# Optimization experiments

Hardware: AMD Instinct MI355X
Metric: run time of the kernel (lower is better)

Reference implementation:

```python
import jax, jax.numpy as jnp
import numpy as np

GAMMA = 0.3
R_PERCENT = 0.2
LAMBDA_PENALTY = 0.5
EPS = 1e-06

B_SZ, N_HEADS, K_FULL = 16, 32, 32768
K_IMG = 16384


def _zscore(x):
    mu = x.mean(axis=-1, keepdims=True)
    std = jnp.sqrt(((x - mu) ** 2).mean(axis=-1, keepdims=True))  # unbiased=False
    return (x - mu) / (std + EPS)


def _topk_binary(scores, k):
    # scores: [B,H] -> binary mask [B,H]; only strictly-positive topk values count
    vals, idx = jax.lax.top_k(scores, k)
    b = jnp.arange(scores.shape[0])[:, None]
    return jnp.zeros_like(scores).at[b, idx].set((vals > 0).astype(scores.dtype))


def setup_inputs() -> dict:
    key = jax.random.key(0)
    k1, k2, k3, k4, k5 = jax.random.split(key, 5)
    attn_logits_last = jax.random.normal(k1, (B_SZ, N_HEADS, K_FULL), dtype=jnp.float32)
    # exactly K_IMG image tokens per row (alternating pattern -> strided gather)
    image_mask = jnp.tile((jnp.arange(K_FULL) % 2 == 0).astype(jnp.int32)[None, :], (B_SZ, 1))
    feat_C = jax.random.normal(k2, (B_SZ, K_IMG), dtype=jnp.float32)
    feat_A = jax.random.normal(k3, (B_SZ, K_IMG), dtype=jnp.float32)
    feat_D = jax.random.normal(k4, (B_SZ, K_IMG), dtype=jnp.float32)
    feat_B = jax.random.normal(k5, (B_SZ, K_IMG), dtype=jnp.float32)
    return {"attn_logits_last": attn_logits_last, "image_mask": image_mask,
            "feat_C": feat_C, "feat_A": feat_A, "feat_D": feat_D, "feat_B": feat_B}


def reference(attn_logits_last, image_mask, feat_C, feat_A, feat_D, feat_B):
    B, H, K_full = attn_logits_last.shape
    K_img = feat_C.shape[1]

    # --- compute_rf ---
    C_t = jax.nn.relu(_zscore(feat_C))
    A_t = jax.nn.sigmoid(_zscore(feat_A))
    D_t = jax.nn.sigmoid(_zscore(feat_D))
    B_t = jax.nn.sigmoid(_zscore(feat_B))
    denom = jnp.maximum(1.0 + LAMBDA_PENALTY * (D_t + B_t), EPS)
    rf = jnp.maximum(C_t * A_t / denom, 0.0)  # [B,K_img]

    # --- align: positions of image tokens (exactly K_img ones per row) ---
    idx = jax.vmap(lambda m: jnp.nonzero(m, size=K_img)[0])(image_mask)  # [B,K_img]

    # --- image-normalized attention ---
    probs_full = jax.nn.softmax(attn_logits_last, axis=-1)
    mask_f = image_mask[:, None, :].astype(attn_logits_last.dtype)  # [B,1,K_full]
    probs_img = probs_full * mask_f
    probs_img_norm = probs_img / jnp.maximum(probs_img.sum(axis=-1, keepdims=True), EPS)
    attn_img_norm = jnp.take_along_axis(probs_img_norm, idx[:, None, :], axis=-1)  # [B,H,K_img]

    # --- dynamic head roles ---
    low_rf = jnp.maximum(1.0 - rf, 0.0)
    s_pos = (attn_img_norm * rf[:, None, :]).sum(axis=-1)   # [B,H]
    s_neg = (attn_img_norm * low_rf[:, None, :]).sum(axis=-1)
    k_heads = min(max(1, int(np.ceil(R_PERCENT * H))), H)
    m_pos = _topk_binary(s_pos, k_heads)
    neg_scores = jnp.where(m_pos > 0, -jnp.inf, s_neg)
    m_neg = _topk_binary(neg_scores, k_heads) * (m_pos == 0).astype(s_pos.dtype)

    # --- delta and scatter back to full logits ---
    delta_img = GAMMA * (m_pos[:, :, None] * rf[:, None, :]
                         - m_neg[:, :, None] * low_rf[:, None, :])  # [B,H,K_img]
    delta_full = jax.vmap(
        lambda d, i: jnp.zeros((H, K_full), attn_logits_last.dtype).at[:, i].set(d)
    )(delta_img, idx)
    delta_full = delta_full * mask_f
    return attn_logits_last + delta_full
```

## Files before the change

kernel.cpp:

```cpp
#include <hip/hip_runtime.h>
#include <math.h>

#define GAMMA 0.3f
#define EPS 1e-6f
#define B_SZ 16
#define NH 32
#define KF 32768
#define KI 16384
#define KHEADS 7

constexpr int OFF_MU    = 0;
constexpr int OFF_SD    = 64;
constexpr int OFF_RAWS  = 128;
constexpr int OFF_RAWP  = 640;
constexpr int OFF_RAWN  = 1152;
constexpr int IOFF_BSUM = 1664;
constexpr int OFF_RFF   = 4096;


__global__ __launch_bounds__(256) void k_stats_cnt(const float* __restrict__ fC,
        const float* __restrict__ fA, const float* __restrict__ fD,
        const float* __restrict__ fB, const int* __restrict__ mask,
        float* __restrict__ ws) {
    __shared__ double r1[256], r2[256];
    __shared__ int sred[256];
    int bid = blockIdx.x, t = threadIdx.x;
    if (bid < 64) {
        int b = bid >> 2, f = bid & 3;
        const float* src;
        if (f == 0) src = fC; else if (f == 1) src = fA; else if (f == 2) src = fD; else src = fB;
        src += (size_t)b * KI;
        double s = 0.0, s2 = 0.0;
        for (int i = t; i < KI / 4; i += 256) {
            float4 v = ((const float4*)src)[i];
            s  += (double)v.x + (double)v.y + (double)v.z + (double)v.w;
            s2 += (double)v.x * v.x + (double)v.y * v.y + (double)v.z * v.z + (double)v.w * v.w;
        }
        r1[t] = s; r2[t] = s2; __syncthreads();
        for (int off = 128; off > 0; off >>= 1) {
            if (t < off) { r1[t] += r1[t + off]; r2[t] += r2[t + off]; }
            __syncthreads();
        }
        if (t == 0) {
            double mu  = r1[0] * (1.0 / KI);
            double var = fmax(r2[0] * (1.0 / KI) - mu * mu, 0.0);
            ws[OFF_MU + bid] = (float)mu;
            ws[OFF_SD + bid] = (float)(sqrt(var) + (double)EPS);
        }
    } else {
        int cblk = bid - 64;
        if (cblk < 6) ws[OFF_RAWS + cblk * 256 + t] = 0.f;
        const int* mrow = mask + (size_t)cblk * 2048;
        int4 m0 = *(const int4*)(mrow + t * 8);
        int4 m1 = *(const int4*)(mrow + t * 8 + 4);
        int cnt = (m0.x != 0) + (m0.y != 0) + (m0.z != 0) + (m0.w != 0)
                + (m1.x != 0) + (m1.y != 0) + (m1.z != 0) + (m1.w != 0);
        sred[t] = cnt; __syncthreads();
        for (int off = 128; off > 0; off >>= 1) {
            if (t < off) sred[t] += sred[t + off];
            __syncthreads();
        }
        if (t == 0) ((int*)ws)[IOFF_BSUM + cblk] = sred[0];
    }
}

__global__ __launch_bounds__(256) void k_rf_expand(const float* __restrict__ fC,
        const float* __restrict__ fA, const float* __restrict__ fD,
        const float* __restrict__ fB, const int* __restrict__ mask,
        float* __restrict__ ws) {
    __shared__ int sc[256];
    __shared__ float rfbuf[2048];
    int blk = blockIdx.x, t = threadIdx.x;
    int b = blk >> 4, c = blk & 15;
    const int* bsum = (const int*)ws + IOFF_BSUM;
    int boff = 0;
    for (int i = 0; i < c; ++i) boff += bsum[(b << 4) + i];
    const int* mrow = mask + (size_t)blk * 2048;
    int4 m0 = *(const int4*)(mrow + t * 8);
    int4 m1 = *(const int4*)(mrow + t * 8 + 4);
    int mv[8] = {m0.x, m0.y, m0.z, m0.w, m1.x, m1.y, m1.z, m1.w};
    int cnt = 0;
    #pragma unroll
    for (int j = 0; j < 8; ++j) cnt += (mv[j] != 0);
    sc[t] = cnt; __syncthreads();
    for (int off = 1; off < 256; off <<= 1) {
        int v = (t >= off) ? sc[t - off] : 0;
        __syncthreads();
        sc[t] += v;
        __syncthreads();
    }
    int total = sc[255];
    int rloc = sc[t] - cnt;
    float mu0 = ws[OFF_MU + b * 4 + 0], sd0 = ws[OFF_SD + b * 4 + 0];
    float mu1 = ws[OFF_MU + b * 4 + 1], sd1 = ws[OFF_SD + b * 4 + 1];
    float mu2 = ws[OFF_MU + b * 4 + 2], sd2 = ws[OFF_SD + b * 4 + 2];
    float mu3 = ws[OFF_MU + b * 4 + 3], sd3 = ws[OFF_SD + b * 4 + 3];
    for (int j = t; j < total; j += 256) {
        size_t idx = (size_t)b * KI + boff + j;
        float Ct = fmaxf((fC[idx] - mu0) / sd0, 0.f);
        float At = 1.f / (1.f + __expf(-((fA[idx] - mu1) / sd1)));
        float Dt = 1.f / (1.f + __expf(-((fD[idx] - mu2) / sd2)));
        float Bt = 1.f / (1.f + __expf(-((fB[idx] - mu3) / sd3)));
        float denom = fmaxf(1.f + 0.5f * (Dt + Bt), EPS);
        rfbuf[j] = fmaxf(Ct * At / denom, 0.f);
    }
    __syncthreads();
    float vr[8];
    #pragma unroll
    for (int j = 0; j < 8; ++j) {
        if (mv[j]) { vr[j] = rfbuf[rloc]; ++rloc; }
        else       { vr[j] = -1.f; }
    }
    float* rff = ws + OFF_RFF + (size_t)blk * 2048 + t * 8;
    *(float4*)(rff)     = *(float4*)(vr);
    *(float4*)(rff + 4) = *(float4*)(vr + 4);
}

__global__ __launch_bounds__(256) void k_scores(const float* __restrict__ attn,
                                                float* __restrict__ ws) {
    int g = blockIdx.x, t = threadIdx.x;
    int bh = g >> 1, half = g & 1;
    int b = bh >> 5;
    const float* xr  = attn + ((size_t)bh << 15) + ((size_t)half << 14);
    const float* rff = ws + OFF_RFF + ((size_t)b << 15) + ((size_t)half << 14);
    float S = 0.f, P = 0.f, N = 0.f;
    #pragma unroll 4
    for (int i = 0; i < 16; ++i) {
        int k = (i * 256 + t) * 4;
        float4 xs = *(const float4*)(xr + k);
        float4 rv = *(const float4*)(rff + k);
        float xa[4] = {xs.x, xs.y, xs.z, xs.w};
        float va[4] = {rv.x, rv.y, rv.z, rv.w};
        #pragma unroll
        for (int j = 0; j < 4; ++j) {
            float e = __expf(xa[j]);
            bool on = va[j] >= 0.f;
            float rfv  = fmaxf(va[j], 0.f);
            float lrfv = on ? fmaxf(1.f - va[j], 0.f) : 0.f;
            S += on ? e : 0.f;
            P = fmaf(e, rfv, P);
            N = fmaf(e, lrfv, N);
        }
    }
    __shared__ float rs[256], rp[256], rn[256];
    rs[t] = S; rp[t] = P; rn[t] = N;
    __syncthreads();
    for (int off = 128; off > 0; off >>= 1) {
        if (t < off) { rs[t] += rs[t + off]; rp[t] += rp[t + off]; rn[t] += rn[t + off]; }
        __syncthreads();
    }
    if (t == 0) {
        atomicAdd(&ws[OFF_RAWS + bh], rs[0]);
        atomicAdd(&ws[OFF_RAWP + bh], rp[0]);
        atomicAdd(&ws[OFF_RAWN + bh], rn[0]);
    }
}

__global__ __launch_bounds__(256) void k_out(const float* __restrict__ attn,
        const float* __restrict__ ws, float* __restrict__ out) {
    unsigned int t = threadIdx.x;
    unsigned int flat = blockIdx.x * 2048 + t * 8;
    unsigned int bh = flat >> 15;
    unsigned int b  = bh >> 5;
    unsigned int h  = bh & 31;

    __shared__ float ssp[NH], snv[NH];
    __shared__ int smp[NH];
    __shared__ float s_gp, s_gn;
    if (t < NH) {
        float S0 = ws[OFF_RAWS + b * NH + t];
        ssp[t] = ws[OFF_RAWP + b * NH + t] / S0;
        snv[t] = ws[OFF_RAWN + b * NH + t] / S0;
    }
    __syncthreads();
    if (t < NH) {
        float sp = ssp[t];
        int cnt = 0;
        for (int j = 0; j < NH; ++j) { float o = ssp[j]; cnt += (o > sp) || (o == sp && j < (int)t); }
        smp[t] = (cnt < KHEADS) && (sp > 0.f);
    }
    __syncthreads();
    if (t < NH && smp[t]) snv[t] = -INFINITY;
    __syncthreads();
    if (t == 0) {
        float gp = 0.f, gn = 0.f;
        if (smp[h]) gp = GAMMA;
        else {
            float nv = snv[h];
            int cnt = 0;
            for (int j = 0; j < NH; ++j) { float o = snv[j]; cnt += (o > nv) || (o == nv && j < (int)h); }
            if ((cnt < KHEADS) && (nv > 0.f)) gn = GAMMA;
        }
        s_gp = gp; s_gn = gn;
    }
    __syncthreads();

    float gp = s_gp, gn = s_gn;
    const float* rff = ws + OFF_RFF + ((size_t)b << 15);
    unsigned int k = flat & (KF - 1);
    #pragma unroll
    for (int half8 = 0; half8 < 2; ++half8) {
        unsigned int f2 = flat + half8 * 4, k2 = k + half8 * 4;
        float4 xs = *(const float4*)(attn + f2);
        float4 rv = *(const float4*)(rff + k2);
        float va[4] = {rv.x, rv.y, rv.z, rv.w};
        float xa[4] = {xs.x, xs.y, xs.z, xs.w};
        float oa[4];
        #pragma unroll
        for (int j = 0; j < 4; ++j) {
            bool on = va[j] >= 0.f;
            float rfv  = fmaxf(va[j], 0.f);
            float lrfv = on ? fmaxf(1.f - va[j], 0.f) : 0.f;
            oa[j] = xa[j] + gp * rfv - gn * lrfv;
        }
        float4 o = {oa[0], oa[1], oa[2], oa[3]};
        *(float4*)(out + f2) = o;
    }
}

extern "C" void kernel_launch(void* const* d_in, const int* in_sizes, int n_in,
                              void* d_out, int out_size, void* d_ws, size_t ws_size,
                              hipStream_t stream) {
    const float* attn = (const float*)d_in[0];
    const int*   mask = (const int*)d_in[1];
    const float* fC   = (const float*)d_in[2];
    const float* fA   = (const float*)d_in[3];
    const float* fD   = (const float*)d_in[4];
    const float* fB   = (const float*)d_in[5];
    float* out = (float*)d_out;
    float* ws = (float*)d_ws;

    k_stats_cnt<<<320, 256, 0, stream>>>(fC, fA, fD, fB, mask, ws);
    k_rf_expand<<<256, 256, 0, stream>>>(fC, fA, fD, fB, mask, ws);
    k_scores   <<<1024, 256, 0, stream>>>(attn, ws);
    k_out      <<<B_SZ * NH * KF / 2048, 256, 0, stream>>>(attn, ws, out);
}
```

Baseline: 149.9 us.

## Use wave shuffle reductions, split score blocks finer, remap output blocks, nontemporal stores

Replaces the shared-memory tree reductions and scans in every kernel with 64-lane shuffle reductions plus a small cross-wave combine, cutting barriers. The scores kernel now uses four blocks per row instead of two, which doubles parallelism but also doubles the atomics. The output kernel permutes its block-to-chunk mapping, likely for cache or channel locality, and writes results with nontemporal stores to avoid polluting the cache. All of this is memory-bound tuning; the block remap could change L2 reuse of the rf buffer either way.

After: 147.2 us, median of 2. About the same (-1.8%).

```diff
diff --git a/kernel.cpp b/kernel.cpp
--- a/kernel.cpp
+++ b/kernel.cpp
@@ -9,6 +9,8 @@
 #define KI 16384
 #define KHEADS 7
 
+typedef float f4v __attribute__((ext_vector_type(4)));
+
 constexpr int OFF_MU    = 0;
 constexpr int OFF_SD    = 64;
 constexpr int OFF_RAWS  = 128;
@@ -22,28 +24,33 @@
         const float* __restrict__ fA, const float* __restrict__ fD,
         const float* __restrict__ fB, const int* __restrict__ mask,
         float* __restrict__ ws) {
-    __shared__ double r1[256], r2[256];
-    __shared__ int sred[256];
     int bid = blockIdx.x, t = threadIdx.x;
+    int lane = t & 63, wid = t >> 6;
     if (bid < 64) {
         int b = bid >> 2, f = bid & 3;
         const float* src;
         if (f == 0) src = fC; else if (f == 1) src = fA; else if (f == 2) src = fD; else src = fB;
         src += (size_t)b * KI;
         double s = 0.0, s2 = 0.0;
+        #pragma unroll 4
         for (int i = t; i < KI / 4; i += 256) {
             float4 v = ((const float4*)src)[i];
             s  += (double)v.x + (double)v.y + (double)v.z + (double)v.w;
             s2 += (double)v.x * v.x + (double)v.y * v.y + (double)v.z * v.z + (double)v.w * v.w;
         }
-        r1[t] = s; r2[t] = s2; __syncthreads();
-        for (int off = 128; off > 0; off >>= 1) {
-            if (t < off) { r1[t] += r1[t + off]; r2[t] += r2[t + off]; }
-            __syncthreads();
-        }
+        #pragma unroll
+        for (int off = 32; off > 0; off >>= 1) {
+            s  += __shfl_down(s, off);
+            s2 += __shfl_down(s2, off);
+        }
+        __shared__ double w1[4], w2[4];
+        if (lane == 0) { w1[wid] = s; w2[wid] = s2; }
+        __syncthreads();
         if (t == 0) {
-            double mu  = r1[0] * (1.0 / KI);
-            double var = fmax(r2[0] * (1.0 / KI) - mu * mu, 0.0);
+            double S1 = w1[0] + w1[1] + w1[2] + w1[3];
+            double S2 = w2[0] + w2[1] + w2[2] + w2[3];
+            double mu  = S1 * (1.0 / KI);
+            double var = fmax(S2 * (1.0 / KI) - mu * mu, 0.0);
             ws[OFF_MU + bid] = (float)mu;
             ws[OFF_SD + bid] = (float)(sqrt(var) + (double)EPS);
         }
@@ -55,12 +62,12 @@
         int4 m1 = *(const int4*)(mrow + t * 8 + 4);
         int cnt = (m0.x != 0) + (m0.y != 0) + (m0.z != 0) + (m0.w != 0)
                 + (m1.x != 0) + (m1.y != 0) + (m1.z != 0) + (m1.w != 0);
-        sred[t] = cnt; __syncthreads();
-        for (int off = 128; off > 0; off >>= 1) {
-            if (t < off) sred[t] += sred[t + off];
-            __syncthreads();
-        }
-        if (t == 0) ((int*)ws)[IOFF_BSUM + cblk] = sred[0];
+        #pragma unroll
+        for (int off = 32; off > 0; off >>= 1) cnt += __shfl_down(cnt, off);
+        __shared__ int wc[4];
+        if (lane == 0) wc[wid] = cnt;
+        __syncthreads();
+        if (t == 0) ((int*)ws)[IOFF_BSUM + cblk] = wc[0] + wc[1] + wc[2] + wc[3];
     }
 }
 
@@ -68,13 +75,16 @@
         const float* __restrict__ fA, const float* __restrict__ fD,
         const float* __restrict__ fB, const int* __restrict__ mask,
         float* __restrict__ ws) {
-    __shared__ int sc[256];
+    __shared__ int sb[16];
+    __shared__ int wsum[4];
     __shared__ float rfbuf[2048];
     int blk = blockIdx.x, t = threadIdx.x;
     int b = blk >> 4, c = blk & 15;
+    int lane = t & 63, wid = t >> 6;
+
     const int* bsum = (const int*)ws + IOFF_BSUM;
-    int boff = 0;
-    for (int i = 0; i < c; ++i) boff += bsum[(b << 4) + i];
+    if (t < 16) sb[t] = (t < c) ? bsum[(b << 4) + t] : 0;
+
     const int* mrow = mask + (size_t)blk * 2048;
     int4 m0 = *(const int4*)(mrow + t * 8);
     int4 m1 = *(const int4*)(mrow + t * 8 + 4);
@@ -82,15 +92,24 @@
     int cnt = 0;
     #pragma unroll
     for (int j = 0; j < 8; ++j) cnt += (mv[j] != 0);
-    sc[t] = cnt; __syncthreads();
-    for (int off = 1; off < 256; off <<= 1) {
-        int v = (t >= off) ? sc[t - off] : 0;
-        __syncthreads();
-        sc[t] += v;
-        __syncthreads();
-    }
-    int total = sc[255];
-    int rloc = sc[t] - cnt;
+
+    int x = cnt;
+    #pragma unroll
+    for (int off = 1; off < 64; off <<= 1) {
+        int v = __shfl_up(x, off);
+        if (lane >= off) x += v;
+    }
+    if (lane == 63) wsum[wid] = x;
+    __syncthreads();
+    int base = 0;
+    #pragma unroll
+    for (int w = 0; w < 4; ++w) base += (w < wid) ? wsum[w] : 0;
+    int total = wsum[0] + wsum[1] + wsum[2] + wsum[3];
+    int rloc = base + x - cnt;
+    int boff = 0;
+    #pragma unroll
+    for (int i = 0; i < 16; ++i) boff += sb[i];
+
     float mu0 = ws[OFF_MU + b * 4 + 0], sd0 = ws[OFF_SD + b * 4 + 0];
     float mu1 = ws[OFF_MU + b * 4 + 1], sd1 = ws[OFF_SD + b * 4 + 1];
     float mu2 = ws[OFF_MU + b * 4 + 2], sd2 = ws[OFF_SD + b * 4 + 2];
@@ -119,13 +138,13 @@
 __global__ __launch_bounds__(256) void k_scores(const float* __restrict__ attn,
                                                 float* __restrict__ ws) {
     int g = blockIdx.x, t = threadIdx.x;
-    int bh = g >> 1, half = g & 1;
+    int bh = g >> 2, qtr = g & 3;
     int b = bh >> 5;
-    const float* xr  = attn + ((size_t)bh << 15) + ((size_t)half << 14);
-    const float* rff = ws + OFF_RFF + ((size_t)b << 15) + ((size_t)half << 14);
+    const float* xr  = attn + ((size_t)bh << 15) + ((size_t)qtr << 13);
+    const float* rff = ws + OFF_RFF + ((size_t)b << 15) + ((size_t)qtr << 13);
     float S = 0.f, P = 0.f, N = 0.f;
-    #pragma unroll 4
-    for (int i = 0; i < 16; ++i) {
+    #pragma unroll
+    for (int i = 0; i < 8; ++i) {
         int k = (i * 256 + t) * 4;
         float4 xs = *(const float4*)(xr + k);
         float4 rv = *(const float4*)(rff + k);
@@ -142,24 +161,30 @@
             N = fmaf(e, lrfv, N);
         }
     }
-    __shared__ float rs[256], rp[256], rn[256];
-    rs[t] = S; rp[t] = P; rn[t] = N;
-    __syncthreads();
-    for (int off = 128; off > 0; off >>= 1) {
-        if (t < off) { rs[t] += rs[t + off]; rp[t] += rp[t + off]; rn[t] += rn[t + off]; }
-        __syncthreads();
-    }
+    int lane = t & 63, wid = t >> 6;
+    #pragma unroll
+    for (int off = 32; off > 0; off >>= 1) {
+        S += __shfl_down(S, off);
+        P += __shfl_down(P, off);
+        N += __shfl_down(N, off);
+    }
+    __shared__ float wS[4], wP[4], wN[4];
+    if (lane == 0) { wS[wid] = S; wP[wid] = P; wN[wid] = N; }
+    __syncthreads();
     if (t == 0) {
-        atomicAdd(&ws[OFF_RAWS + bh], rs[0]);
-        atomicAdd(&ws[OFF_RAWP + bh], rp[0]);
-        atomicAdd(&ws[OFF_RAWN + bh], rn[0]);
+        atomicAdd(&ws[OFF_RAWS + bh], wS[0] + wS[1] + wS[2] + wS[3]);
+        atomicAdd(&ws[OFF_RAWP + bh], wP[0] + wP[1] + wP[2] + wP[3]);
+        atomicAdd(&ws[OFF_RAWN + bh], wN[0] + wN[1] + wN[2] + wN[3]);
     }
 }
 
 __global__ __launch_bounds__(256) void k_out(const float* __restrict__ attn,
         const float* __restrict__ ws, float* __restrict__ out) {
     unsigned int t = threadIdx.x;
-    unsigned int flat = blockIdx.x * 2048 + t * 8;
+    unsigned int j = blockIdx.x;
+    unsigned int r = j & 7, q = j >> 3;
+    unsigned int chunk = 8u * r + 64u * (q >> 3) + (q & 7);
+    unsigned int flat = chunk * 2048 + t * 8;
     unsigned int bh = flat >> 15;
     unsigned int b  = bh >> 5;
     unsigned int h  = bh & 31;
@@ -176,7 +201,7 @@
     if (t < NH) {
         float sp = ssp[t];
         int cnt = 0;
-        for (int j = 0; j < NH; ++j) { float o = ssp[j]; cnt += (o > sp) || (o == sp && j < (int)t); }
+        for (int jj = 0; jj < NH; ++jj) { float o = ssp[jj]; cnt += (o > sp) || (o == sp && jj < (int)t); }
         smp[t] = (cnt < KHEADS) && (sp > 0.f);
     }
     __syncthreads();
@@ -188,7 +213,7 @@
         else {
             float nv = snv[h];
             int cnt = 0;
-            for (int j = 0; j < NH; ++j) { float o = snv[j]; cnt += (o > nv) || (o == nv && j < (int)h); }
+            for (int jj = 0; jj < NH; ++jj) { float o = snv[jj]; cnt += (o > nv) || (o == nv && jj < (int)h); }
             if ((cnt < KHEADS) && (nv > 0.f)) gn = GAMMA;
         }
         s_gp = gp; s_gn = gn;
@@ -207,14 +232,14 @@
         float xa[4] = {xs.x, xs.y, xs.z, xs.w};
         float oa[4];
         #pragma unroll
-        for (int j = 0; j < 4; ++j) {
-            bool on = va[j] >= 0.f;
-            float rfv  = fmaxf(va[j], 0.f);
-            float lrfv = on ? fmaxf(1.f - va[j], 0.f) : 0.f;
-            oa[j] = xa[j] + gp * rfv - gn * lrfv;
-        }
-        float4 o = {oa[0], oa[1], oa[2], oa[3]};
-        *(float4*)(out + f2) = o;
+        for (int jj = 0; jj < 4; ++jj) {
+            bool on = va[jj] >= 0.f;
+            float rfv  = fmaxf(va[jj], 0.f);
+            float lrfv = on ? fmaxf(1.f - va[jj], 0.f) : 0.f;
+            oa[jj] = xa[jj] + gp * rfv - gn * lrfv;
+        }
+        f4v o = {oa[0], oa[1], oa[2], oa[3]};
+        __builtin_nontemporal_store(o, (f4v*)(out + f2));
     }
 }
 
@@ -232,6 +257,6 @@
 
     k_stats_cnt<<<320, 256, 0, stream>>>(fC, fA, fD, fB, mask, ws);
     k_rf_expand<<<256, 256, 0, stream>>>(fC, fA, fD, fB, mask, ws);
-    k_scores   <<<1024, 256, 0, stream>>>(attn, ws);
+    k_scores   <<<2048, 256, 0, stream>>>(attn, ws);
     k_out      <<<B_SZ * NH * KF / 2048, 256, 0, stream>>>(attn, ws, out);
 }
```
